# Performance work log

Hardware: AMD Instinct MI355X
Metric: run time of the kernel (lower is better)

## Reference

```python
import jax, jax.numpy as jnp
import numpy as np

N = 100000
E = 1600000
D_IN = 128
D_H = 128
BN_EPS = 1e-5


def setup_inputs() -> dict:
    key = jax.random.key(0)
    ks = jax.random.split(key, 8)
    x = jax.random.normal(ks[0], (N, D_IN), dtype=jnp.float32)
    edge_index = jax.random.randint(ks[1], (2, E), 0, N, dtype=jnp.int64)
    # MLP params (Linear stores weight as [out, in])
    lim1 = 1.0 / np.sqrt(D_IN)
    W1 = jax.random.uniform(ks[2], (D_H, D_IN), minval=-lim1, maxval=lim1, dtype=jnp.float32)
    b1 = jax.random.uniform(ks[3], (D_H,), minval=-lim1, maxval=lim1, dtype=jnp.float32)
    gamma = jnp.ones((D_H,), dtype=jnp.float32)
    beta = jnp.zeros((D_H,), dtype=jnp.float32)
    lim2 = 1.0 / np.sqrt(D_H)
    W2 = jax.random.uniform(ks[4], (D_H, D_H), minval=-lim2, maxval=lim2, dtype=jnp.float32)
    b2 = jax.random.uniform(ks[5], (D_H,), minval=-lim2, maxval=lim2, dtype=jnp.float32)
    eps = jnp.float32(0.0)  # trainable eps parameter, init 0
    return {"x": x, "edge_index": edge_index, "eps": eps, "W1": W1, "b1": b1,
            "gamma": gamma, "beta": beta, "W2": W2, "b2": b2}


def reference(x, edge_index, eps, W1, b1, gamma, beta, W2, b2):
    src = edge_index[0]
    dst = edge_index[1]
    # Augmented edges = original + reversed + self-loops.
    # aggr[dst] += x[src]; aggr[src] += x[dst]; aggr[i] += x[i]
    aggr = jnp.zeros_like(x).at[dst].add(x[src]).at[src].add(x[dst]) + x
    h = (1.0 + eps) * x + aggr              # [N, D_IN]
    h = h @ W1.T + b1                        # [N, D_H]
    # BatchNorm1d in training mode: batch stats, biased variance
    mean = jnp.mean(h, axis=0)
    var = jnp.mean(jnp.square(h - mean), axis=0)
    h = gamma * (h - mean) * jax.lax.rsqrt(var + BN_EPS) + beta
    h = jax.nn.relu(h)
    return h @ W2.T + b2                     # [N, D_H]
```

## Files before the change

kernel.cpp:

```cpp
#include <hip/hip_runtime.h>
#include <hip/hip_fp16.h>

#define N_NODES 100000
#define EDGES   1600000
#define D       128
#define BN_EPS  1e-5f
#define TM      64
#define NT      ((N_NODES + TM - 1) / TM)
#define GGRID   782
#define NB      782
#define SLOT    4800
#define L1E     8
#define L1TILE  (256 * L1E)
#define GBLKS   1536
#define GWAVES  (GBLKS * 4)
#define NREP    32

typedef __attribute__((ext_vector_type(8))) short short8;
typedef __attribute__((ext_vector_type(4))) float f32x4;

__device__ __forceinline__ unsigned short bf_hi(float f) {
    unsigned u = __float_as_uint(f);
    unsigned t = u + 0x7FFF + ((u >> 16) & 1);
    return (unsigned short)(t >> 16);
}
__device__ __forceinline__ float bf_val(unsigned short h) {
    return __uint_as_float(((unsigned)h) << 16);
}

__global__ void zero_split(int* __restrict__ zbase,
                           const float* __restrict__ W1, const float* __restrict__ W2,
                           unsigned short* __restrict__ w1h, unsigned short* __restrict__ w1l,
                           unsigned short* __restrict__ w2h, unsigned short* __restrict__ w2l) {
    int gid = blockIdx.x * blockDim.x + threadIdx.x;
    if (gid < 9216) zbase[gid] = 0;
    if (gid < 16384) {
        float f = W1[gid];
        unsigned short h = bf_hi(f);
        w1h[gid] = h;
        w1l[gid] = bf_hi(f - bf_val(h));
    } else {
        int j = gid - 16384;
        float f = W2[j];
        unsigned short h = bf_hi(f);
        w2h[j] = h;
        w2l[j] = bf_hi(f - bf_val(h));
    }
}

__launch_bounds__(256)
__global__ void fused_pg(const float* __restrict__ x,
                         const unsigned short* __restrict__ w1h,
                         const unsigned short* __restrict__ w1l,
                         __half* __restrict__ yh,
                         const int* __restrict__ ei, int* __restrict__ gcur,
                         int* __restrict__ pairs) {
    __shared__ unsigned short sH[TM][136];
    __shared__ unsigned short sL[TM][136];
    const int tid = threadIdx.x;

    if (blockIdx.x >= GGRID) {
        int* cnt   = (int*)&sH[0][0];
        int* cbase = cnt + NB;
        for (int i = tid; i < NB; i += 256) cnt[i] = 0;
        __syncthreads();

        int bbA[L1E], rrA[L1E], pkA[L1E];
        int bbB[L1E], rrB[L1E], pkB[L1E];
        const int t0 = (blockIdx.x - GGRID) * L1TILE + tid;
#pragma unroll
        for (int j = 0; j < L1E; ++j) {
            int t = t0 + j * 256;
            bbA[j] = -1;
            bbB[j] = -1;
            if (t < EDGES) {
                int s = ei[t];
                int d = ei[EDGES + t];
                bbA[j] = d >> 7;
                pkA[j] = ((d & 127) << 17) | s;
                rrA[j] = atomicAdd(&cnt[bbA[j]], 1);
                bbB[j] = s >> 7;
                pkB[j] = ((s & 127) << 17) | d;
                rrB[j] = atomicAdd(&cnt[bbB[j]], 1);
            }
        }
        __syncthreads();
        for (int i = tid; i < NB; i += 256) {
            int c = cnt[i];
            cbase[i] = c ? (i * SLOT + atomicAdd(&gcur[i], c)) : 0;
        }
        __syncthreads();
#pragma unroll
        for (int j = 0; j < L1E; ++j) {
            if (bbA[j] >= 0) {
                pairs[cbase[bbA[j]] + rrA[j]] = pkA[j];
                pairs[cbase[bbB[j]] + rrB[j]] = pkB[j];
            }
        }
        return;
    }

    const int wv  = tid >> 6;
    const int ln  = tid & 63;
    const int lc  = ln & 15;
    const int qd  = ln >> 4;
    const int sr  = tid >> 5;
    const int sc4 = tid & 31;

    short8 Bh[4][2], Bl[4][2];
#pragma unroll
    for (int kk = 0; kk < 4; ++kk)
#pragma unroll
        for (int tl = 0; tl < 2; ++tl) {
            int woff = (wv * 32 + tl * 16 + lc) * D + kk * 32 + qd * 8;
            Bh[kk][tl] = *(const short8*)(w1h + woff);
            Bl[kk][tl] = *(const short8*)(w1l + woff);
        }

    float4 pf[8];
    int tile = blockIdx.x;
#pragma unroll
    for (int i = 0; i < 8; ++i) {
        int gr = tile * TM + sr + i * 8;
        pf[i] = make_float4(0.f, 0.f, 0.f, 0.f);
        if (gr < N_NODES)
            pf[i] = *(const float4*)(x + (long long)gr * D + sc4 * 4);
    }

    while (tile < NT) {
#pragma unroll
        for (int i = 0; i < 8; ++i) {
            float4 v = pf[i];
            unsigned short h0 = bf_hi(v.x), h1b = bf_hi(v.y), h2 = bf_hi(v.z), h3 = bf_hi(v.w);
            unsigned short l0 = bf_hi(v.x - bf_val(h0)), l1 = bf_hi(v.y - bf_val(h1b));
            unsigned short l2 = bf_hi(v.z - bf_val(h2)), l3 = bf_hi(v.w - bf_val(h3));
            int r = sr + i * 8;
            *(uint2*)&sH[r][sc4 * 4] = make_uint2((unsigned)h0 | ((unsigned)h1b << 16),
                                                  (unsigned)h2 | ((unsigned)h3 << 16));
            *(uint2*)&sL[r][sc4 * 4] = make_uint2((unsigned)l0 | ((unsigned)l1 << 16),
                                                  (unsigned)l2 | ((unsigned)l3 << 16));
        }
        __syncthreads();
        int nxt = tile + GGRID;
        if (nxt < NT) {
#pragma unroll
            for (int i = 0; i < 8; ++i) {
                int gr = nxt * TM + sr + i * 8;
                pf[i] = make_float4(0.f, 0.f, 0.f, 0.f);
                if (gr < N_NODES)
                    pf[i] = *(const float4*)(x + (long long)gr * D + sc4 * 4);
            }
        }

        f32x4 acc[4][2];
#pragma unroll
        for (int m = 0; m < 4; ++m)
#pragma unroll
            for (int tl = 0; tl < 2; ++tl) acc[m][tl] = (f32x4){0.f, 0.f, 0.f, 0.f};

#pragma unroll
        for (int kk = 0; kk < 4; ++kk) {
#pragma unroll
            for (int m = 0; m < 4; ++m) {
                short8 ah = *(const short8*)&sH[m * 16 + lc][kk * 32 + qd * 8];
                short8 al = *(const short8*)&sL[m * 16 + lc][kk * 32 + qd * 8];
#pragma unroll
                for (int tl = 0; tl < 2; ++tl) {
                    acc[m][tl] = __builtin_amdgcn_mfma_f32_16x16x32_bf16(ah, Bh[kk][tl], acc[m][tl], 0, 0, 0);
                    acc[m][tl] = __builtin_amdgcn_mfma_f32_16x16x32_bf16(al, Bh[kk][tl], acc[m][tl], 0, 0, 0);
                    acc[m][tl] = __builtin_amdgcn_mfma_f32_16x16x32_bf16(ah, Bl[kk][tl], acc[m][tl], 0, 0, 0);
                }
            }
        }

        const int row0 = tile * TM;
#pragma unroll
        for (int m = 0; m < 4; ++m)
#pragma unroll
            for (int tl = 0; tl < 2; ++tl) {
                int col = wv * 32 + tl * 16 + lc;
#pragma unroll
                for (int r = 0; r < 4; ++r) {
                    int grow = row0 + m * 16 + qd * 4 + r;
                    if (grow < N_NODES)
                        yh[(long long)grow * D + col] = __float2half(acc[m][tl][r]);
                }
            }
        __syncthreads();
        tile = nxt;
    }
}

__launch_bounds__(256)
__global__ void bucket_fill(int* __restrict__ pairs, const int* __restrict__ gcur,
                            int* __restrict__ ofs, int* __restrict__ oen) {
    __shared__ int sP[SLOT];
    __shared__ int lc[128];
    __shared__ int cur[128];
    const int b    = blockIdx.x;
    const int tid  = threadIdx.x;
    const int base = b * SLOT;
    const int m    = min(gcur[b], SLOT);
    for (int i = tid; i < m; i += 256) sP[i] = pairs[base + i];
    if (tid < 128) lc[tid] = 0;
    __syncthreads();
    for (int i = tid; i < m; i += 256) atomicAdd(&lc[sP[i] >> 17], 1);
    __syncthreads();
    int v = (tid < 128) ? lc[tid] : 0;
    for (int d = 1; d < 128; d <<= 1) {
        int u = (tid >= d && tid < 128) ? lc[tid - d] : 0;
        __syncthreads();
        if (tid < 128) lc[tid] += u;
        __syncthreads();
    }
    if (tid < 128) {
        int abs0 = base + lc[tid] - v;
        cur[tid] = abs0;
        const int n = (b << 7) + tid;
        if (n < N_NODES) { ofs[n] = abs0; oen[n] = abs0 + v; }
    }
    __syncthreads();
    for (int i = tid; i < m; i += 256) {
        int p = sP[i];
        int r = atomicAdd(&cur[p >> 17], 1);
        pairs[r] = p & 0x1FFFF;
    }
}

__launch_bounds__(256)
__global__ void gather_aggr(const __half* __restrict__ yh,
                            const int* __restrict__ adj, const int* __restrict__ ofs,
                            const int* __restrict__ oen, const float* __restrict__ eps_p,
                            const float* __restrict__ b1,
                            float* __restrict__ h1, float* __restrict__ stats) {
    const int wv   = threadIdx.x >> 6;
    const int lane = threadIdx.x & 63;
    const int wave = blockIdx.x * 4 + wv;
    const __half2* xp = (const __half2*)yh;
    const float sc = 2.0f + eps_p[0];
    const float2 b1c = ((const float2*)b1)[lane];
    float sx = 0.f, sy = 0.f, qx = 0.f, qy = 0.f;

    for (int node = wave; node < N_NODES; node += GWAVES) {
        int b = ofs[node];
        int e = oen[node];
        float ax = 0.f, ay = 0.f;
        int i = b;
        for (; i + 8 <= e; i += 8) {
            int n0 = adj[i],     n1 = adj[i + 1], n2 = adj[i + 2], n3 = adj[i + 3];
            int n4 = adj[i + 4], n5 = adj[i + 5], n6 = adj[i + 6], n7 = adj[i + 7];
            __half2 v0 = xp[(unsigned)n0 * 64u + lane];
            __half2 v1 = xp[(unsigned)n1 * 64u + lane];
            __half2 v2 = xp[(unsigned)n2 * 64u + lane];
            __half2 v3 = xp[(unsigned)n3 * 64u + lane];
            __half2 v4 = xp[(unsigned)n4 * 64u + lane];
            __half2 v5 = xp[(unsigned)n5 * 64u + lane];
            __half2 v6 = xp[(unsigned)n6 * 64u + lane];
            __half2 v7 = xp[(unsigned)n7 * 64u + lane];
            float2 f0 = __half22float2(v0);
            float2 f1 = __half22float2(v1);
            float2 f2 = __half22float2(v2);
            float2 f3 = __half22float2(v3);
            float2 f4 = __half22float2(v4);
            float2 f5 = __half22float2(v5);
            float2 f6 = __half22float2(v6);
            float2 f7 = __half22float2(v7);
            ax += ((f0.x + f1.x) + (f2.x + f3.x)) + ((f4.x + f5.x) + (f6.x + f7.x));
            ay += ((f0.y + f1.y) + (f2.y + f3.y)) + ((f4.y + f5.y) + (f6.y + f7.y));
        }
        for (; i + 4 <= e; i += 4) {
            int n0 = adj[i], n1 = adj[i + 1], n2 = adj[i + 2], n3 = adj[i + 3];
            __half2 v0 = xp[(unsigned)n0 * 64u + lane];
            __half2 v1 = xp[(unsigned)n1 * 64u + lane];
            __half2 v2 = xp[(unsigned)n2 * 64u + lane];
            __half2 v3 = xp[(unsigned)n3 * 64u + lane];
            float2 f0 = __half22float2(v0);
            float2 f1 = __half22float2(v1);
            float2 f2 = __half22float2(v2);
            float2 f3 = __half22float2(v3);
            ax += (f0.x + f1.x) + (f2.x + f3.x);
            ay += (f0.y + f1.y) + (f2.y + f3.y);
        }
        for (; i < e; ++i) {
            __half2 v = xp[(unsigned)adj[i] * 64u + lane];
            float2 f = __half22float2(v);
            ax += f.x;
            ay += f.y;
        }
        float2 ys = __half22float2(xp[(unsigned)node * 64u + lane]);
        float ox = fmaf(sc, ys.x, ax) + b1c.x;
        float oy = fmaf(sc, ys.y, ay) + b1c.y;
        ((float2*)h1)[(long long)node * 64 + lane] = make_float2(ox, oy);
        sx += ox; sy += oy;
        qx += ox * ox; qy += oy * oy;
    }

    __shared__ float4 red[4][64];
    red[wv][lane] = make_float4(sx, sy, qx, qy);
    __syncthreads();
    if (wv == 0) {
        float4 a = red[0][lane], b4 = red[1][lane], c = red[2][lane], d4 = red[3][lane];
        float fx = (a.x + b4.x) + (c.x + d4.x);
        float fy = (a.y + b4.y) + (c.y + d4.y);
        float gx = (a.z + b4.z) + (c.z + d4.z);
        float gy = (a.w + b4.w) + (c.w + d4.w);
        float* st = stats + (blockIdx.x & (NREP - 1)) * 256;
        atomicAdd(&st[2 * lane],       fx);
        atomicAdd(&st[2 * lane + 1],   fy);
        atomicAdd(&st[128 + 2 * lane],     gx);
        atomicAdd(&st[128 + 2 * lane + 1], gy);
    }
}

__launch_bounds__(256)
__global__ void gemm2_mfma(float* __restrict__ h1out,
                           const unsigned short* __restrict__ w2h,
                           const unsigned short* __restrict__ w2l,
                           const float* __restrict__ b2, const float* __restrict__ stats,
                           const float* __restrict__ gamma, const float* __restrict__ beta) {
    __shared__ unsigned short sH[TM][136];
    __shared__ unsigned short sL[TM][136];
    __shared__ float sScale[128];
    __shared__ float sShift[128];
    const int tid = threadIdx.x;
    const int wv  = tid >> 6;
    const int ln  = tid & 63;
    const int lc  = ln & 15;
    const int qd  = ln >> 4;
    const int sr  = tid >> 5;
    const int sc4 = tid & 31;

    if (tid < 128) {
        float s = 0.f, q = 0.f;
#pragma unroll
        for (int r = 0; r < NREP; ++r) {
            s += stats[r * 256 + tid];
            q += stats[r * 256 + 128 + tid];
        }
        float mean = s * (1.0f / N_NODES);
        float var  = fmaxf(q * (1.0f / N_NODES) - mean * mean, 0.0f);
        float sc   = gamma[tid] * rsqrtf(var + BN_EPS);
        sScale[tid] = sc;
        sShift[tid] = beta[tid] - mean * sc;
    }

    short8 Bh[4][2], Bl[4][2];
#pragma unroll
    for (int kk = 0; kk < 4; ++kk)
#pragma unroll
        for (int tl = 0; tl < 2; ++tl) {
            int woff = (wv * 32 + tl * 16 + lc) * D + kk * 32 + qd * 8;
            Bh[kk][tl] = *(const short8*)(w2h + woff);
            Bl[kk][tl] = *(const short8*)(w2l + woff);
        }
    float bb[2];
    bb[0] = b2[wv * 32 + lc];
    bb[1] = b2[wv * 32 + 16 + lc];

    __syncthreads();

    float4 pf[8];
    int tile = blockIdx.x;
#pragma unroll
    for (int i = 0; i < 8; ++i) {
        int gr = tile * TM + sr + i * 8;
        pf[i] = make_float4(0.f, 0.f, 0.f, 0.f);
        if (gr < N_NODES)
            pf[i] = *(const float4*)(h1out + (long long)gr * D + sc4 * 4);
    }

    while (tile < NT) {
        float4 scv = *(const float4*)&sScale[sc4 * 4];
        float4 shv = *(const float4*)&sShift[sc4 * 4];
#pragma unroll
        for (int i = 0; i < 8; ++i) {
            int gr = tile * TM + sr + i * 8;
            float4 v = pf[i];
            if (gr < N_NODES) {
                v.x = fmaxf(0.f, fmaf(v.x, scv.x, shv.x));
                v.y = fmaxf(0.f, fmaf(v.y, scv.y, shv.y));
                v.z = fmaxf(0.f, fmaf(v.z, scv.z, shv.z));
                v.w = fmaxf(0.f, fmaf(v.w, scv.w, shv.w));
            } else {
                v = make_float4(0.f, 0.f, 0.f, 0.f);
            }
            unsigned short h0 = bf_hi(v.x), h1b = bf_hi(v.y), h2 = bf_hi(v.z), h3 = bf_hi(v.w);
            unsigned short l0 = bf_hi(v.x - bf_val(h0)), l1 = bf_hi(v.y - bf_val(h1b));
            unsigned short l2 = bf_hi(v.z - bf_val(h2)), l3 = bf_hi(v.w - bf_val(h3));
            int r = sr + i * 8;
            *(uint2*)&sH[r][sc4 * 4] = make_uint2((unsigned)h0 | ((unsigned)h1b << 16),
                                                  (unsigned)h2 | ((unsigned)h3 << 16));
            *(uint2*)&sL[r][sc4 * 4] = make_uint2((unsigned)l0 | ((unsigned)l1 << 16),
                                                  (unsigned)l2 | ((unsigned)l3 << 16));
        }
        __syncthreads();
        int nxt = tile + GGRID;
        if (nxt < NT) {
#pragma unroll
            for (int i = 0; i < 8; ++i) {
                int gr = nxt * TM + sr + i * 8;
                pf[i] = make_float4(0.f, 0.f, 0.f, 0.f);
                if (gr < N_NODES)
                    pf[i] = *(const float4*)(h1out + (long long)gr * D + sc4 * 4);
            }
        }

        f32x4 acc[4][2];
#pragma unroll
        for (int m = 0; m < 4; ++m)
#pragma unroll
            for (int tl = 0; tl < 2; ++tl) acc[m][tl] = (f32x4){0.f, 0.f, 0.f, 0.f};

#pragma unroll
        for (int kk = 0; kk < 4; ++kk) {
#pragma unroll
            for (int m = 0; m < 4; ++m) {
                short8 ah = *(const short8*)&sH[m * 16 + lc][kk * 32 + qd * 8];
                short8 al = *(const short8*)&sL[m * 16 + lc][kk * 32 + qd * 8];
#pragma unroll
                for (int tl = 0; tl < 2; ++tl) {
                    acc[m][tl] = __builtin_amdgcn_mfma_f32_16x16x32_bf16(ah, Bh[kk][tl], acc[m][tl], 0, 0, 0);
                    acc[m][tl] = __builtin_amdgcn_mfma_f32_16x16x32_bf16(al, Bh[kk][tl], acc[m][tl], 0, 0, 0);
                    acc[m][tl] = __builtin_amdgcn_mfma_f32_16x16x32_bf16(ah, Bl[kk][tl], acc[m][tl], 0, 0, 0);
                }
            }
        }

        const int row0 = tile * TM;
#pragma unroll
        for (int m = 0; m < 4; ++m)
#pragma unroll
            for (int tl = 0; tl < 2; ++tl) {
                int col = wv * 32 + tl * 16 + lc;
#pragma unroll
                for (int r = 0; r < 4; ++r) {
                    int grow = row0 + m * 16 + qd * 4 + r;
                    if (grow < N_NODES)
                        h1out[(long long)grow * D + col] = acc[m][tl][r] + bb[tl];
                }
            }
        __syncthreads();
        tile = nxt;
    }
}

extern "C" void kernel_launch(void* const* d_in, const int* in_sizes, int n_in,
                              void* d_out, int out_size, void* d_ws, size_t ws_size,
                              hipStream_t stream) {
    const float* x     = (const float*)d_in[0];
    const int*   ei    = (const int*)d_in[1];
    const float* eps_p = (const float*)d_in[2];
    const float* W1    = (const float*)d_in[3];
    const float* b1    = (const float*)d_in[4];
    const float* gamma = (const float*)d_in[5];
    const float* beta  = (const float*)d_in[6];
    const float* W2    = (const float*)d_in[7];
    const float* b2    = (const float*)d_in[8];

    __half* yh   = (__half*)d_ws;
    float*  stats = (float*)(yh + (long long)N_NODES * D);
    int*    gcur  = (int*)(stats + NREP * 256);
    int*    ofs   = gcur + 1024;
    int*    oen   = ofs + N_NODES;
    unsigned short* w1h = (unsigned short*)(oen + N_NODES);
    unsigned short* w1l = w1h + 16384;
    unsigned short* w2h = w1l + 16384;
    unsigned short* w2l = w2h + 16384;
    int*    pairs = (int*)(w2l + 16384);
    int*    adj   = pairs;

    float* out = (float*)d_out;

    {
        zero_split<<<128, 256, 0, stream>>>((int*)stats, W1, W2, w1h, w1l, w2h, w2l);
    }
    {
        fused_pg<<<GGRID + 782, 256, 0, stream>>>(x, w1h, w1l, yh, ei, gcur, pairs);
    }
    {
        bucket_fill<<<NB, 256, 0, stream>>>(pairs, gcur, ofs, oen);
    }
    {
        gather_aggr<<<GBLKS, 256, 0, stream>>>(yh, adj, ofs, oen, eps_p, b1, out, stats);
    }
    {
        gemm2_mfma<<<GGRID, 256, 0, stream>>>(out, w2h, w2l, b2, stats, gamma, beta);
    }
}
```

Measured before the change: 329.9 us.

## Inline weight bf16 splitting into GEMMs and sub-bucket adjacency by source

Removes the separate zero_split kernel: weights are now split into bf16 hi/lo parts on the fly inside each GEMM kernel, and zeroing uses hipMemsetAsync. bucket_fill now counting-sorts each destination's neighbor list into 13 sub-buckets by source ID range, so the gather reads source rows in a more localized order. This trades one launch and a workspace round trip for redundant per-block weight conversion, and adds extra shared-memory counters and scan work in bucket_fill to improve cache locality of the gather.

New measurement: 338.1 us. 2.5% more time.

```diff
diff --git a/kernel.cpp b/kernel.cpp
--- a/kernel.cpp
+++ b/kernel.cpp
@@ -10,6 +10,7 @@
 #define GGRID   782
 #define NB      782
 #define SLOT    4800
+#define SBS     13
 #define L1E     8
 #define L1TILE  (256 * L1E)
 #define GBLKS   1536
@@ -27,31 +28,21 @@
 __device__ __forceinline__ float bf_val(unsigned short h) {
     return __uint_as_float(((unsigned)h) << 16);
 }
-
-__global__ void zero_split(int* __restrict__ zbase,
-                           const float* __restrict__ W1, const float* __restrict__ W2,
-                           unsigned short* __restrict__ w1h, unsigned short* __restrict__ w1l,
-                           unsigned short* __restrict__ w2h, unsigned short* __restrict__ w2l) {
-    int gid = blockIdx.x * blockDim.x + threadIdx.x;
-    if (gid < 9216) zbase[gid] = 0;
-    if (gid < 16384) {
-        float f = W1[gid];
-        unsigned short h = bf_hi(f);
-        w1h[gid] = h;
-        w1l[gid] = bf_hi(f - bf_val(h));
-    } else {
-        int j = gid - 16384;
-        float f = W2[j];
-        unsigned short h = bf_hi(f);
-        w2h[j] = h;
-        w2l[j] = bf_hi(f - bf_val(h));
-    }
+__device__ __forceinline__ void split8(const float* __restrict__ p, short8* hi, short8* lo) {
+    short8 h, l;
+#pragma unroll
+    for (int i = 0; i < 8; ++i) {
+        float f = p[i];
+        unsigned short hh = bf_hi(f);
+        ((unsigned short*)&h)[i] = (short)hh;
+        ((unsigned short*)&l)[i] = (short)bf_hi(f - bf_val(hh));
+    }
+    *hi = h; *lo = l;
 }
 
 __launch_bounds__(256)
 __global__ void fused_pg(const float* __restrict__ x,
-                         const unsigned short* __restrict__ w1h,
-                         const unsigned short* __restrict__ w1l,
+                         const float* __restrict__ W1,
                          __half* __restrict__ yh,
                          const int* __restrict__ ei, int* __restrict__ gcur,
                          int* __restrict__ pairs) {
@@ -113,8 +104,7 @@
 #pragma unroll
         for (int tl = 0; tl < 2; ++tl) {
             int woff = (wv * 32 + tl * 16 + lc) * D + kk * 32 + qd * 8;
-            Bh[kk][tl] = *(const short8*)(w1h + woff);
-            Bl[kk][tl] = *(const short8*)(w1l + woff);
+            split8(W1 + woff, &Bh[kk][tl], &Bl[kk][tl]);
         }
 
     float4 pf[8];
@@ -195,18 +185,27 @@
 __global__ void bucket_fill(int* __restrict__ pairs, const int* __restrict__ gcur,
                             int* __restrict__ ofs, int* __restrict__ oen) {
     __shared__ int sP[SLOT];
+    __shared__ int cnt2[128 * SBS];
     __shared__ int lc[128];
-    __shared__ int cur[128];
     const int b    = blockIdx.x;
     const int tid  = threadIdx.x;
     const int base = b * SLOT;
     const int m    = min(gcur[b], SLOT);
     for (int i = tid; i < m; i += 256) sP[i] = pairs[base + i];
-    if (tid < 128) lc[tid] = 0;
-    __syncthreads();
-    for (int i = tid; i < m; i += 256) atomicAdd(&lc[sP[i] >> 17], 1);
-    __syncthreads();
-    int v = (tid < 128) ? lc[tid] : 0;
+    for (int i = tid; i < 128 * SBS; i += 256) cnt2[i] = 0;
+    __syncthreads();
+    for (int i = tid; i < m; i += 256) {
+        int p = sP[i];
+        atomicAdd(&cnt2[(p >> 17) * SBS + ((p & 0x1FFFF) >> 13)], 1);
+    }
+    __syncthreads();
+    int v = 0;
+    if (tid < 128) {
+#pragma unroll
+        for (int j = 0; j < SBS; ++j) v += cnt2[tid * SBS + j];
+        lc[tid] = v;
+    }
+    __syncthreads();
     for (int d = 1; d < 128; d <<= 1) {
         int u = (tid >= d && tid < 128) ? lc[tid - d] : 0;
         __syncthreads();
@@ -214,16 +213,22 @@
         __syncthreads();
     }
     if (tid < 128) {
-        int abs0 = base + lc[tid] - v;
-        cur[tid] = abs0;
+        int run = base + lc[tid] - v;
         const int n = (b << 7) + tid;
-        if (n < N_NODES) { ofs[n] = abs0; oen[n] = abs0 + v; }
+        if (n < N_NODES) { ofs[n] = run; oen[n] = run + v; }
+#pragma unroll
+        for (int j = 0; j < SBS; ++j) {
+            int c = cnt2[tid * SBS + j];
+            cnt2[tid * SBS + j] = run;
+            run += c;
+        }
     }
     __syncthreads();
     for (int i = tid; i < m; i += 256) {
         int p = sP[i];
-        int r = atomicAdd(&cur[p >> 17], 1);
-        pairs[r] = p & 0x1FFFF;
+        int src = p & 0x1FFFF;
+        int r = atomicAdd(&cnt2[(p >> 17) * SBS + (src >> 13)], 1);
+        pairs[r] = src;
     }
 }
 
@@ -314,8 +319,7 @@
 
 __launch_bounds__(256)
 __global__ void gemm2_mfma(float* __restrict__ h1out,
-                           const unsigned short* __restrict__ w2h,
-                           const unsigned short* __restrict__ w2l,
+                           const float* __restrict__ W2,
                            const float* __restrict__ b2, const float* __restrict__ stats,
                            const float* __restrict__ gamma, const float* __restrict__ beta) {
     __shared__ unsigned short sH[TM][136];
@@ -350,8 +354,7 @@
 #pragma unroll
         for (int tl = 0; tl < 2; ++tl) {
             int woff = (wv * 32 + tl * 16 + lc) * D + kk * 32 + qd * 8;
-            Bh[kk][tl] = *(const short8*)(w2h + woff);
-            Bl[kk][tl] = *(const short8*)(w2l + woff);
+            split8(W2 + woff, &Bh[kk][tl], &Bl[kk][tl]);
         }
     float bb[2];
     bb[0] = b2[wv * 32 + lc];
@@ -462,20 +465,15 @@
     int*    gcur  = (int*)(stats + NREP * 256);
     int*    ofs   = gcur + 1024;
     int*    oen   = ofs + N_NODES;
-    unsigned short* w1h = (unsigned short*)(oen + N_NODES);
-    unsigned short* w1l = w1h + 16384;
-    unsigned short* w2h = w1l + 16384;
-    unsigned short* w2l = w2h + 16384;
-    int*    pairs = (int*)(w2l + 16384);
+    int*    pairs = (int*)(oen + N_NODES);
     int*    adj   = pairs;
 
     float* out = (float*)d_out;
 
+    hipMemsetAsync(stats, 0, (NREP * 256 + 1024) * sizeof(int), stream);
+
     {
-        zero_split<<<128, 256, 0, stream>>>((int*)stats, W1, W2, w1h, w1l, w2h, w2l);
-    }
-    {
-        fused_pg<<<GGRID + 782, 256, 0, stream>>>(x, w1h, w1l, yh, ei, gcur, pairs);
+        fused_pg<<<GGRID + 782, 256, 0, stream>>>(x, W1, yh, ei, gcur, pairs);
     }
     {
         bucket_fill<<<NB, 256, 0, stream>>>(pairs, gcur, ofs, oen);
@@ -484,6 +482,6 @@
         gather_aggr<<<GBLKS, 256, 0, stream>>>(yh, adj, ofs, oen, eps_p, b1, out, stats);
     }
     {
-        gemm2_mfma<<<GGRID, 256, 0, stream>>>(out, w2h, w2l, b2, stats, gamma, beta);
-    }
-}
+        gemm2_mfma<<<GGRID, 256, 0, stream>>>(out, W2, b2, stats, gamma, beta);
+    }
+}
```
